# Kernel optimization log

Measured on AMD Instinct MI355X. Metric: run time of the kernel, lower is better.

Reference implementation:

```python
import jax, jax.numpy as jnp
import numpy as np

SIGMA2_MU = 0.5  # hyper_params['sigma2_mu']
R = 128          # number of spatial basis functions
NV = 2000        # number of query points
KM1 = 30         # K - 1


def setup_inputs() -> dict:
    key = jax.random.key(0)
    k1, k2, k3, k4 = jax.random.split(key, 4)
    Xi_evals = jax.random.normal(k1, (R, NV), dtype=jnp.float32)
    vec_W_post_mean = jax.random.normal(k2, (R * KM1, 1), dtype=jnp.float32)
    vec_W_post_cov = jax.random.normal(k3, (R * KM1, R * KM1), dtype=jnp.float32)
    C_mu = jax.random.normal(k4, (NV, 1), dtype=jnp.float32)
    return {"Xi_evals": Xi_evals, "vec_W_post_mean": vec_W_post_mean,
            "vec_W_post_cov": vec_W_post_cov, "C_mu": C_mu}


def reference(Xi_evals, vec_W_post_mean, vec_W_post_cov, C_mu):
    # Xi_evals: (r, Nv); vec_W_post_mean: (r*(K-1), 1); vec_W_post_cov: (r*(K-1), r*(K-1))
    r, Nv = Xi_evals.shape
    Km1 = vec_W_post_mean.shape[0] // r
    K = Km1 + 1
    X = Xi_evals.T                                # (Nv, r)
    # kron(x^T, I_{K-1}) @ w  ==  X @ W  with W = w.reshape(r, K-1)
    W = vec_W_post_mean.reshape(r, Km1)
    Post_mean_c = X @ W                           # (Nv, K-1)
    # kron(x^T, I) @ Cov @ kron(x, I): quadratic form over r-blocks
    C4 = vec_W_post_cov.reshape(r, Km1, r, Km1)   # (i, k, j, l)
    A = jnp.einsum('vi,ikjl->vkjl', X, C4)        # (Nv, K-1, r, K-1)
    Post_cov_c = jnp.einsum('vkjl,vj->vkl', A, X) # (Nv, K-1, K-1)
    Post_mean_coefs = jnp.concatenate([C_mu, Post_mean_c], axis=1)  # (Nv, K)
    Post_cov_mats = jnp.zeros((Nv, K, K), dtype=Xi_evals.dtype)
    Post_cov_mats = Post_cov_mats.at[:, 0, 0].set(SIGMA2_MU)
    Post_cov_mats = Post_cov_mats.at[:, 1:, 1:].set(Post_cov_c)
    return Post_mean_coefs, Post_cov_mats
```

## Files before the change

### kernel.cpp

```cpp
#include <hip/hip_runtime.h>

typedef _Float16 f16;
typedef _Float16 f16x8 __attribute__((ext_vector_type(8)));
typedef float    f32x16 __attribute__((ext_vector_type(16)));

#define NV      2000
#define RR      128
#define KM1     30
#define KKOUT   31
#define NQ      900
#define QQ      961
#define COV_OFF 62000

#define B2_BYTES 31457280

#define PERM_BLKS  3840
#define XCAST_BLKS 128
#define ZERO_BLKS  1877
#define MEAN_BLKS  248
#define PREP_GRID  (PERM_BLKS + XCAST_BLKS + ZERO_BLKS + MEAN_BLKS)

__global__ void prep_kernel(const float* __restrict__ Xi,
                            const float* __restrict__ Wm,
                            const float* __restrict__ cov,
                            const float* __restrict__ Cmu,
                            f16* __restrict__ B2,
                            f16* __restrict__ Xh,
                            float* __restrict__ outm,
                            float* __restrict__ oc) {
    int b = blockIdx.x;
    if (b < PERM_BLKS) {
        __shared__ float row[3840];
        int i = b / 30, k = b - i * 30;
        const float4* src4 = (const float4*)(cov + (size_t)b * 3840);
        for (int t = threadIdx.x; t < 960; t += 256)
            *(float4*)&row[t * 4] = src4[t];
        __syncthreads();
#pragma unroll
        for (int it = 0; it < 2; ++it) {
            int t = threadIdx.x + it * 256;
            int s = t >> 6, kq = (t >> 5) & 1, ql = t & 31;
            if (ql < 30) {
                int q = 30 * k + ql;
                int qt = q >> 5, l31 = q & 31;
                const float* rp = row + (s * 16 + kq * 8) * 30 + ql;
                f16 vals[8];
#pragma unroll
                for (int d = 0; d < 8; ++d) vals[d] = (f16)rp[d * 30];
                f16* dst = B2 + (((size_t)qt * 128 + i) * 8 + s) * 512 + kq * 256 + l31 * 8;
                *(uint4*)dst = *(uint4*)vals;
            }
        }
        return;
    }
    b -= PERM_BLKS;
    if (b < XCAST_BLKS) {
        int t = b * 256 + threadIdx.x;
        int v = t & 2047, rc = t >> 11;
        f16 vals[8];
#pragma unroll
        for (int d = 0; d < 8; ++d) {
            float x = (v < NV) ? Xi[(rc * 8 + d) * NV + v] : 0.f;
            vals[d] = (f16)x;
        }
        *(uint4*)(Xh + (size_t)v * 128 + rc * 8) = *(uint4*)vals;
        return;
    }
    b -= XCAST_BLKS;
    if (b < ZERO_BLKS) {
        size_t idx = ((size_t)b * 256 + threadIdx.x) * 4;
        if (idx < (size_t)NV * QQ) {
            unsigned rem = (unsigned)(idx % QQ);
            float4 zv;
            zv.x = (rem == 0u)   ? 0.5f : 0.f;
            zv.y = (rem == 960u) ? 0.5f : 0.f;
            zv.z = (rem == 959u) ? 0.5f : 0.f;
            zv.w = (rem == 958u) ? 0.5f : 0.f;
            *(float4*)(oc + idx) = zv;
        }
        return;
    }
    b -= ZERO_BLKS;
    int tid = b * 256 + threadIdx.x;
    int c = tid >> 11;
    int v = tid & 2047;
    if (v >= NV || c >= KKOUT) return;
    if (c == 0) { outm[(size_t)v * KKOUT] = Cmu[v]; return; }
    float acc = 0.f;
    const float* w = Wm + (c - 1);
#pragma unroll 8
    for (int i = 0; i < RR; ++i)
        acc = fmaf(Xi[i * NV + v], w[i * KM1], acc);
    outm[(size_t)v * KKOUT + c] = acc;
}

__launch_bounds__(256, 2)
__global__ void gemm_cov3_kernel(const f16* __restrict__ B2,
                                 const f16* __restrict__ Xh,
                                 float* __restrict__ out_cov) {
    const int bid = blockIdx.x;
    const int S = ((bid >> 6) << 3) + (bid & 7);
    if (S >= 60) return;
    const int y  = (bid >> 3) & 7;
    const int z  = S / 30;
    const int qt = S - z * 30;

    const int tid  = threadIdx.x;
    const int lane = tid & 63;
    const int wm   = tid >> 6;
    const int l31  = lane & 31, kq = lane >> 5;
    const int v0   = y * 256;

    const int vr0 = v0 + wm * 64 + l31;
    const f16* xrow0 = Xh + (size_t)vr0 * 128;
    const f16* xrow1 = xrow0 + 32 * 128;

    f16x8 xj[2][8];
#pragma unroll
    for (int s = 0; s < 8; ++s) {
        xj[0][s] = *(const f16x8*)(xrow0 + s * 16 + kq * 8);
        xj[1][s] = *(const f16x8*)(xrow1 + s * 16 + kq * 8);
    }

    const int ibeg = z * 64;
    const f16* bptr = B2 + ((size_t)qt * 128 + ibeg) * 4096 + lane * 8;

    f32x16 acc[2] = {};
    f16x8 bbuf[2][8];
#pragma unroll
    for (int s = 0; s < 8; ++s)
        bbuf[0][s] = *(const f16x8*)(bptr + s * 512);

    for (int g = 0; g < 8; ++g) {
        f16x8 xi0 = *(const f16x8*)(xrow0 + ibeg + g * 8);
        f16x8 xi1 = *(const f16x8*)(xrow1 + ibeg + g * 8);
#pragma unroll
        for (int t = 0; t < 8; ++t) {
            const int st = g * 8 + t;
            const int p  = t & 1;
            const f16* nb = bptr + (size_t)(st < 63 ? st + 1 : 63) * 4096;
#pragma unroll
            for (int s = 0; s < 8; ++s)
                bbuf[p ^ 1][s] = *(const f16x8*)(nb + s * 512);
            f16 a0 = xi0[t], a1 = xi1[t];
            f16x8 xs0, xs1;
#pragma unroll
            for (int d = 0; d < 8; ++d) { xs0[d] = a0; xs1[d] = a1; }
#pragma unroll
            for (int s = 0; s < 8; ++s) {
                f16x8 af0 = xs0 * xj[0][s];
                f16x8 af1 = xs1 * xj[1][s];
                acc[0] = __builtin_amdgcn_mfma_f32_32x32x16_f16(af0, bbuf[p][s], acc[0], 0, 0, 0);
                acc[1] = __builtin_amdgcn_mfma_f32_32x32x16_f16(af1, bbuf[p][s], acc[1], 0, 0, 0);
            }
        }
    }

    const int q = qt * 32 + l31;
    if (q >= NQ) return;
    const int kk = q / 30, ll = q - kk * 30;
    float* cb = out_cov + (kk + 1) * KKOUT + (ll + 1);
#pragma unroll
    for (int fm = 0; fm < 2; ++fm) {
        int vb = v0 + wm * 64 + fm * 32 + 4 * kq;
#pragma unroll
        for (int r = 0; r < 16; ++r) {
            int v = vb + (r & 3) + 8 * (r >> 2);
            if (v < NV) atomicAdd(cb + (size_t)v * QQ, acc[fm][r]);
        }
    }
}

extern "C" void kernel_launch(void* const* d_in, const int* in_sizes, int n_in,
                              void* d_out, int out_size, void* d_ws, size_t ws_size,
                              hipStream_t stream) {
    const float* Xi  = (const float*)d_in[0];
    const float* Wm  = (const float*)d_in[1];
    const float* Cov = (const float*)d_in[2];
    const float* Cmu = (const float*)d_in[3];
    float* out      = (float*)d_out;
    float* out_mean = out;
    float* out_cov  = out + COV_OFF;
    f16* B2 = (f16*)d_ws;
    f16* Xh = (f16*)((char*)d_ws + B2_BYTES);

    prep_kernel     <<<PREP_GRID, 256, 0, stream>>>(Xi, Wm, Cov, Cmu, B2, Xh, out_mean, out_cov);
    gemm_cov3_kernel<<<512, 256, 0, stream>>>(B2, Xh, out_cov);
}
```

Before: 185.4 us.

## Exploit quadratic-form symmetry by folding covariance into upper-triangular block slots

The prep kernel now symmetrizes the covariance over the r index (adds the transposed block into the upper triangle and zeroes below the diagonal at 16-row granularity), then packs only the needed triangular slots into a compact f16 buffer. The GEMM kernel walks variable-length i ranges, skipping lower-triangular j-blocks via templated stages, and uses 4 fragments per wave with a load-balanced split of i into four ranges. This roughly halves the MFMA work and B traffic. In exchange it adds strided gather reads of the transpose in prep, another X layout copy, and the rebalanced tiling drops the double-buffered B prefetch.

```diff
diff --git a/kernel.cpp b/kernel.cpp
--- a/kernel.cpp
+++ b/kernel.cpp
@@ -11,51 +11,71 @@
 #define NQ      900
 #define QQ      961
 #define COV_OFF 62000
-
-#define B2_BYTES 31457280
+#define NSLOT   576
+#define NQT     29
+
+#define B2S_BYTES 17104896
+#define XH_BYTES  524288
+
+__device__ __forceinline__ int slot_base(int i) {
+    int g = i >> 4, r = i & 15;
+    return 16 * (8 * g - (g * (g - 1)) / 2) + r * (8 - g);
+}
 
 #define PERM_BLKS  3840
-#define XCAST_BLKS 128
+#define XC1_BLKS   128
+#define XC2_BLKS   128
 #define ZERO_BLKS  1877
 #define MEAN_BLKS  248
-#define PREP_GRID  (PERM_BLKS + XCAST_BLKS + ZERO_BLKS + MEAN_BLKS)
+#define PREP_GRID  (PERM_BLKS + XC1_BLKS + XC2_BLKS + ZERO_BLKS + MEAN_BLKS)
 
 __global__ void prep_kernel(const float* __restrict__ Xi,
                             const float* __restrict__ Wm,
                             const float* __restrict__ cov,
                             const float* __restrict__ Cmu,
-                            f16* __restrict__ B2,
+                            f16* __restrict__ B2s,
                             f16* __restrict__ Xh,
+                            f16* __restrict__ Xh2,
                             float* __restrict__ outm,
                             float* __restrict__ oc) {
+    __shared__ float rowS[3840];
     int b = blockIdx.x;
+    int tid = threadIdx.x;
     if (b < PERM_BLKS) {
-        __shared__ float row[3840];
         int i = b / 30, k = b - i * 30;
-        const float4* src4 = (const float4*)(cov + (size_t)b * 3840);
-        for (int t = threadIdx.x; t < 960; t += 256)
-            *(float4*)&row[t * 4] = src4[t];
+        int j0 = (i >> 4) << 4;
+        int W = 128 - j0;
+        int lo = (i - j0) * 30;
+        const float* src = cov + (size_t)b * 3840 + j0 * 30;
+        for (int t = tid; t < W * 30; t += 256)
+            rowS[t] = (t >= lo) ? src[t] : 0.f;
         __syncthreads();
-#pragma unroll
-        for (int it = 0; it < 2; ++it) {
-            int t = threadIdx.x + it * 256;
-            int s = t >> 6, kq = (t >> 5) & 1, ql = t & 31;
-            if (ql < 30) {
-                int q = 30 * k + ql;
-                int qt = q >> 5, l31 = q & 31;
-                const float* rp = row + (s * 16 + kq * 8) * 30 + ql;
-                f16 vals[8];
-#pragma unroll
-                for (int d = 0; d < 8; ++d) vals[d] = (f16)rp[d * 30];
-                f16* dst = B2 + (((size_t)qt * 128 + i) * 8 + s) * 512 + kq * 256 + l31 * 8;
-                *(uint4*)dst = *(uint4*)vals;
-            }
+        int n2 = (127 - i) * 30;
+        for (int idx = tid; idx < n2; idx += 256) {
+            int j = i + 1 + idx / 30;
+            int l = idx - (j - i - 1) * 30;
+            rowS[(j - j0) * 30 + l] += cov[(size_t)(j * 30 + k) * 3840 + i * 30 + l];
+        }
+        __syncthreads();
+        int base_i = slot_base(i);
+        int nOct = W >> 3;
+        for (int it = tid; it < nOct * 30; it += 256) {
+            int oct = it / 30, l = it - oct * 30;
+            int j = j0 + oct * 8;
+            int s = j >> 4, kq = (j >> 3) & 1;
+            int q = k * 30 + l, qt = q >> 5, l31 = q & 31;
+            int slot = base_i + s - (i >> 4);
+            f16* dst = B2s + (((size_t)qt * NSLOT + slot) * 64 + kq * 32 + l31) * 8;
+            f16 vals[8];
+#pragma unroll
+            for (int d = 0; d < 8; ++d) vals[d] = (f16)rowS[(j + d - j0) * 30 + l];
+            *(uint4*)dst = *(uint4*)vals;
         }
         return;
     }
     b -= PERM_BLKS;
-    if (b < XCAST_BLKS) {
-        int t = b * 256 + threadIdx.x;
+    if (b < XC1_BLKS) {
+        int t = b * 256 + tid;
         int v = t & 2047, rc = t >> 11;
         f16 vals[8];
 #pragma unroll
@@ -66,9 +86,22 @@
         *(uint4*)(Xh + (size_t)v * 128 + rc * 8) = *(uint4*)vals;
         return;
     }
-    b -= XCAST_BLKS;
+    b -= XC1_BLKS;
+    if (b < XC2_BLKS) {
+        int t = b * 256 + tid;
+        int r = t >> 8, v8 = (t & 255) * 8;
+        f16 vals[8];
+#pragma unroll
+        for (int d = 0; d < 8; ++d) {
+            int v = v8 + d;
+            vals[d] = (f16)((v < NV) ? Xi[r * NV + v] : 0.f);
+        }
+        *(uint4*)(Xh2 + (size_t)r * 2048 + v8) = *(uint4*)vals;
+        return;
+    }
+    b -= XC2_BLKS;
     if (b < ZERO_BLKS) {
-        size_t idx = ((size_t)b * 256 + threadIdx.x) * 4;
+        size_t idx = ((size_t)b * 256 + tid) * 4;
         if (idx < (size_t)NV * QQ) {
             unsigned rem = (unsigned)(idx % QQ);
             float4 zv;
@@ -81,9 +114,8 @@
         return;
     }
     b -= ZERO_BLKS;
-    int tid = b * 256 + threadIdx.x;
-    int c = tid >> 11;
-    int v = tid & 2047;
+    int t2 = b * 256 + tid;
+    int c = t2 >> 11, v = t2 & 2047;
     if (v >= NV || c >= KKOUT) return;
     if (c == 0) { outm[(size_t)v * KKOUT] = Cmu[v]; return; }
     float acc = 0.f;
@@ -94,65 +126,76 @@
     outm[(size_t)v * KKOUT + c] = acc;
 }
 
+template<int G>
+__device__ __forceinline__ void do_stage(const f16*& bptr,
+                                         const f16x8 (&xj)[4][8],
+                                         const f16 (&xi)[4],
+                                         f32x16 (&acc)[4]) {
+    f16x8 bf[8 - G];
+#pragma unroll
+    for (int s = G; s < 8; ++s) { bf[s - G] = *(const f16x8*)bptr; bptr += 512; }
+    f16x8 xs[4];
+#pragma unroll
+    for (int fm = 0; fm < 4; ++fm)
+#pragma unroll
+        for (int d = 0; d < 8; ++d) xs[fm][d] = xi[fm];
+#pragma unroll
+    for (int s = G; s < 8; ++s)
+#pragma unroll
+        for (int fm = 0; fm < 4; ++fm) {
+            f16x8 af = xs[fm] * xj[fm][s];
+            acc[fm] = __builtin_amdgcn_mfma_f32_32x32x16_f16(af, bf[s - G], acc[fm], 0, 0, 0);
+        }
+}
+
 __launch_bounds__(256, 2)
-__global__ void gemm_cov3_kernel(const f16* __restrict__ B2,
-                                 const f16* __restrict__ Xh,
-                                 float* __restrict__ out_cov) {
+__global__ void gemm4_kernel(const f16* __restrict__ B2s,
+                             const f16* __restrict__ Xh,
+                             const f16* __restrict__ Xh2,
+                             float* __restrict__ out_cov) {
     const int bid = blockIdx.x;
-    const int S = ((bid >> 6) << 3) + (bid & 7);
-    if (S >= 60) return;
-    const int y  = (bid >> 3) & 7;
-    const int z  = S / 30;
-    const int qt = S - z * 30;
-
-    const int tid  = threadIdx.x;
-    const int lane = tid & 63;
-    const int wm   = tid >> 6;
-    const int l31  = lane & 31, kq = lane >> 5;
-    const int v0   = y * 256;
-
-    const int vr0 = v0 + wm * 64 + l31;
-    const f16* xrow0 = Xh + (size_t)vr0 * 128;
-    const f16* xrow1 = xrow0 + 32 * 128;
-
-    f16x8 xj[2][8];
-#pragma unroll
-    for (int s = 0; s < 8; ++s) {
-        xj[0][s] = *(const f16x8*)(xrow0 + s * 16 + kq * 8);
-        xj[1][s] = *(const f16x8*)(xrow1 + s * 16 + kq * 8);
-    }
-
-    const int ibeg = z * 64;
-    const f16* bptr = B2 + ((size_t)qt * 128 + ibeg) * 4096 + lane * 8;
-
-    f32x16 acc[2] = {};
-    f16x8 bbuf[2][8];
-#pragma unroll
-    for (int s = 0; s < 8; ++s)
-        bbuf[0][s] = *(const f16x8*)(bptr + s * 512);
-
-    for (int g = 0; g < 8; ++g) {
-        f16x8 xi0 = *(const f16x8*)(xrow0 + ibeg + g * 8);
-        f16x8 xi1 = *(const f16x8*)(xrow1 + ibeg + g * 8);
-#pragma unroll
-        for (int t = 0; t < 8; ++t) {
-            const int st = g * 8 + t;
-            const int p  = t & 1;
-            const f16* nb = bptr + (size_t)(st < 63 ? st + 1 : 63) * 4096;
-#pragma unroll
-            for (int s = 0; s < 8; ++s)
-                bbuf[p ^ 1][s] = *(const f16x8*)(nb + s * 512);
-            f16 a0 = xi0[t], a1 = xi1[t];
-            f16x8 xs0, xs1;
-#pragma unroll
-            for (int d = 0; d < 8; ++d) { xs0[d] = a0; xs1[d] = a1; }
-#pragma unroll
-            for (int s = 0; s < 8; ++s) {
-                f16x8 af0 = xs0 * xj[0][s];
-                f16x8 af1 = xs1 * xj[1][s];
-                acc[0] = __builtin_amdgcn_mfma_f32_32x32x16_f16(af0, bbuf[p][s], acc[0], 0, 0, 0);
-                acc[1] = __builtin_amdgcn_mfma_f32_32x32x16_f16(af1, bbuf[p][s], acc[1], 0, 0, 0);
-            }
+    const int slice = ((bid >> 5) << 3) + (bid & 7);
+    if (slice >= NQT * 4) return;
+    const int qt = slice >> 2, kz = slice & 3;
+    const int ILO[4] = {0, 19, 40, 68};
+    const int IHI[4] = {19, 40, 68, 128};
+    const int SLO[4] = {0, 149, 288, 432};
+
+    const int tid = threadIdx.x, lane = tid & 63, w = tid >> 6;
+    const int l31 = lane & 31, kq = lane >> 5;
+    const int v0 = ((bid >> 3) & 3) * 512 + w * 128;
+    const int vr = v0 + l31;
+
+    f16x8 xj[4][8];
+#pragma unroll
+    for (int fm = 0; fm < 4; ++fm)
+#pragma unroll
+        for (int s = 0; s < 8; ++s)
+            xj[fm][s] = *(const f16x8*)(Xh + (size_t)(vr + fm * 32) * 128 + s * 16 + kq * 8);
+
+    const int ilo = ILO[kz], ihi = IHI[kz];
+    const f16* bptr = B2s + ((size_t)qt * NSLOT + SLO[kz]) * 512 + lane * 8;
+
+    f32x16 acc[4] = {};
+    f16 xi[4], xin[4];
+#pragma unroll
+    for (int fm = 0; fm < 4; ++fm) xin[fm] = Xh2[(size_t)ilo * 2048 + vr + fm * 32];
+
+    for (int i = ilo; i < ihi; ++i) {
+#pragma unroll
+        for (int fm = 0; fm < 4; ++fm) xi[fm] = xin[fm];
+        int inext = (i + 1 < ihi) ? i + 1 : i;
+#pragma unroll
+        for (int fm = 0; fm < 4; ++fm) xin[fm] = Xh2[(size_t)inext * 2048 + vr + fm * 32];
+        switch (i >> 4) {
+            case 0: do_stage<0>(bptr, xj, xi, acc); break;
+            case 1: do_stage<1>(bptr, xj, xi, acc); break;
+            case 2: do_stage<2>(bptr, xj, xi, acc); break;
+            case 3: do_stage<3>(bptr, xj, xi, acc); break;
+            case 4: do_stage<4>(bptr, xj, xi, acc); break;
+            case 5: do_stage<5>(bptr, xj, xi, acc); break;
+            case 6: do_stage<6>(bptr, xj, xi, acc); break;
+            default: do_stage<7>(bptr, xj, xi, acc); break;
         }
     }
 
@@ -161,8 +204,8 @@
     const int kk = q / 30, ll = q - kk * 30;
     float* cb = out_cov + (kk + 1) * KKOUT + (ll + 1);
 #pragma unroll
-    for (int fm = 0; fm < 2; ++fm) {
-        int vb = v0 + wm * 64 + fm * 32 + 4 * kq;
+    for (int fm = 0; fm < 4; ++fm) {
+        int vb = v0 + fm * 32 + 4 * kq;
 #pragma unroll
         for (int r = 0; r < 16; ++r) {
             int v = vb + (r & 3) + 8 * (r >> 2);
@@ -181,9 +224,11 @@
     float* out      = (float*)d_out;
     float* out_mean = out;
     float* out_cov  = out + COV_OFF;
-    f16* B2 = (f16*)d_ws;
-    f16* Xh = (f16*)((char*)d_ws + B2_BYTES);
-
-    prep_kernel     <<<PREP_GRID, 256, 0, stream>>>(Xi, Wm, Cov, Cmu, B2, Xh, out_mean, out_cov);
-    gemm_cov3_kernel<<<512, 256, 0, stream>>>(B2, Xh, out_cov);
-}
+    f16* B2s = (f16*)d_ws;
+    f16* Xh  = (f16*)((char*)d_ws + B2S_BYTES);
+    f16* Xh2 = (f16*)((char*)d_ws + B2S_BYTES + XH_BYTES);
+
+    prep_kernel <<<PREP_GRID, 256, 0, stream>>>(Xi, Wm, Cov, Cmu, B2s, Xh, Xh2,
+                                                out_mean, out_cov);
+    gemm4_kernel<<<480, 256, 0, stream>>>(B2s, Xh, Xh2, out_cov);
+}
```

After: 204.3 us. 10.2% more time.
